# Kernel tuning notes

Measured on AMD Instinct MI355X. Metric: run time of the kernel, lower is better.

Reference implementation:

```python
import jax, jax.numpy as jnp
import numpy as np

OUT_F, IN_F = 4096, 4096
BITS = 4
B, S = 4, 2048


def setup_inputs() -> dict:
    key = jax.random.key(0)
    k_x, k_cb, k_rot, k_b, k_idx = jax.random.split(key, 5)
    x = jax.random.normal(k_x, (B, S, IN_F), dtype=jnp.float32)
    # per-coordinate codebook indices for each weight row (int, constant)
    indices = jax.random.randint(k_idx, (OUT_F, IN_F), 0, 2 ** BITS, dtype=jnp.int32)
    # scalar codebook with 2^bits levels
    codebook = jax.random.normal(k_cb, (2 ** BITS,), dtype=jnp.float32)
    # random rotation Pi (d x d); faithful math only needs it orthogonal-ish
    rotation_matrix = jax.random.normal(k_rot, (IN_F, IN_F), dtype=jnp.float32) / np.sqrt(IN_F)
    bias = jax.random.normal(k_b, (OUT_F,), dtype=jnp.float32)
    return {"x": x, "indices": indices, "codebook": codebook,
            "rotation_matrix": rotation_matrix, "bias": bias}


def reference(x, indices, codebook, rotation_matrix, bias):
    # Dequantize: look up codewords per coordinate in rotated space, then
    # undo the rotation: W = C[idx] @ Pi^T  -> [out_features, in_features]
    rotated = codebook[indices]                      # [O, D] gather
    weight = jnp.einsum('od,kd->ok', rotated, rotation_matrix)  # rotated @ Pi^T
    # F.linear(x, W, bias) = x @ W^T + bias
    out = jnp.einsum('bsd,od->bso', x, weight) + bias
    return out
```

## Files before the change

### kernel.cpp

```cpp
#include <hip/hip_runtime.h>
#include <hip/hip_bf16.h>


typedef __attribute__((ext_vector_type(8))) __bf16 bf16x8;
typedef __attribute__((ext_vector_type(4))) float f32x4;

#define GLOAD_LDS16(g, l)                                                        \
  __builtin_amdgcn_global_load_lds((__attribute__((address_space(1))) void*)(g), \
                                   (__attribute__((address_space(3))) void*)(l), \
                                   16, 0, 0)


__global__ __launch_bounds__(256) void cvt_f32_bf16(const float* __restrict__ in,
                                                    __hip_bfloat16* __restrict__ out, int n4) {
  int i = blockIdx.x * 256 + threadIdx.x;
  if (i >= n4) return;
  float4 v = *(const float4*)(in + (size_t)i * 4);
  union { __hip_bfloat16 h[4]; ushort4 u; } o;
  o.h[0] = __float2bfloat16(v.x);
  o.h[1] = __float2bfloat16(v.y);
  o.h[2] = __float2bfloat16(v.z);
  o.h[3] = __float2bfloat16(v.w);
  *(ushort4*)((unsigned short*)out + (size_t)i * 4) = o.u;
}

__global__ __launch_bounds__(256) void dequant_bf16(const int* __restrict__ idx,
                                                    const float* __restrict__ cb,
                                                    __hip_bfloat16* __restrict__ out, int n4) {
  __shared__ __hip_bfloat16 scb[16];
  if (threadIdx.x < 16) scb[threadIdx.x] = __float2bfloat16(cb[threadIdx.x]);
  __syncthreads();
  int i = blockIdx.x * 256 + threadIdx.x;
  if (i >= n4) return;
  int4 v = *(const int4*)(idx + (size_t)i * 4);
  union { __hip_bfloat16 h[4]; ushort4 u; } o;
  o.h[0] = scb[v.x & 15];
  o.h[1] = scb[v.y & 15];
  o.h[2] = scb[v.z & 15];
  o.h[3] = scb[v.w & 15];
  *(ushort4*)((unsigned short*)out + (size_t)i * 4) = o.u;
}


template <bool OUT_BF16>
__global__ __launch_bounds__(512, 2) void gemm256(const __hip_bfloat16* __restrict__ A,
                                                  const __hip_bfloat16* __restrict__ B,
                                                  void* __restrict__ Cv,
                                                  const float* __restrict__ bias,
                                                  int M, int N, int K) {
  __shared__ __align__(16) char smem[131072];

  const int nbn = N >> 8;
  const int nwg = (M >> 8) * nbn;
  const int bid0 = blockIdx.x;
  const int cpx = nwg >> 3;
  const int bid = (bid0 & 7) * cpx + (bid0 >> 3);
  const int m0 = (bid / nbn) << 8;
  const int n0 = (bid % nbn) << 8;

  const int tid = (int)threadIdx.x;
  const int lane = tid & 63;
  const int w = tid >> 6;
  const int wr = w >> 2;
  const int wc = w & 3;
  const int fr = lane & 15;
  const int fq = lane >> 4;

  const int srow = lane >> 3;
  const int scol = ((lane & 7) ^ srow) << 3;

  const __hip_bfloat16* Ab = A + (size_t)m0 * K;
  const __hip_bfloat16* Bb = B + (size_t)n0 * K;

  const int NT = K >> 6;

  f32x4 acc[8][4];
#pragma unroll
  for (int i = 0; i < 8; ++i)
#pragma unroll
    for (int j = 0; j < 4; ++j) acc[i][j] = (f32x4){0.f, 0.f, 0.f, 0.f};

  auto stage = [&](int s) {
    const int t = s >> 2, kind = s & 3;
    const __hip_bfloat16* g = (kind < 2) ? Ab : Bb;
    char* region = smem + ((kind < 2) ? 0 : 65536) + (t & 1) * 32768 + (kind & 1) * 16384;
    const int grow = (kind & 1) * 128 + w * 16 + srow;
    const int k0 = t << 6;
#pragma unroll
    for (int j = 0; j < 2; ++j)
      GLOAD_LDS16(g + (size_t)(grow + j * 8) * K + (k0 + scol), region + w * 2048 + j * 1024);
  };

  const int sw = (fr & 7) << 4;

  auto ldA = [&](int b, int mh, int mf, int kk) -> bf16x8 {
    const int row = wr * 128 + mh * 64 + mf * 16 + fr;
    const int byte = b * 32768 + row * 128 + ((kk * 64 + fq * 16) ^ sw);
    return *(const bf16x8*)(smem + byte);
  };
  auto ldB = [&](int b, int nf, int kk) -> bf16x8 {
    const int row = wc * 64 + nf * 16 + fr;
    const int byte = 65536 + b * 32768 + row * 128 + ((kk * 64 + fq * 16) ^ sw);
    return *(const bf16x8*)(smem + byte);
  };

  stage(0); stage(1); stage(2); stage(3);
  stage(6); stage(7);
  asm volatile("s_waitcnt vmcnt(4)" ::: "memory");
  __builtin_amdgcn_s_barrier();

  bf16x8 afA[4], afB[4], bk0[4], bk1[4];

  for (int T = 0; T < NT; ++T) {
    const int b = T & 1;
    const bool pf1 = (T + 1 < NT);
    const bool pf2 = (T + 2 < NT);

    if (pf1) stage(4 * (T + 1) + 0);
#pragma unroll
    for (int mf = 0; mf < 4; ++mf) afA[mf] = ldA(b, 0, mf, 0);
#pragma unroll
    for (int nf = 0; nf < 4; ++nf) bk0[nf] = ldB(b, nf, 0);
    __builtin_amdgcn_s_barrier();
    asm volatile("s_waitcnt lgkmcnt(0)");
    __builtin_amdgcn_sched_barrier(0);
#pragma unroll
    for (int mf = 0; mf < 4; ++mf) afB[mf] = ldA(b, 0, mf, 1);
#pragma unroll
    for (int nf = 0; nf < 4; ++nf) bk1[nf] = ldB(b, nf, 1);
    __builtin_amdgcn_s_setprio(1);
#pragma unroll
    for (int nf = 0; nf < 4; ++nf)
#pragma unroll
      for (int mf = 0; mf < 4; ++mf)
        acc[mf][nf] = __builtin_amdgcn_mfma_f32_16x16x32_bf16(afA[mf], bk0[nf], acc[mf][nf], 0, 0, 0);
    __builtin_amdgcn_s_setprio(0);
    __builtin_amdgcn_s_barrier();

    if (pf1) stage(4 * (T + 1) + 1);
    __builtin_amdgcn_s_barrier();
    asm volatile("s_waitcnt lgkmcnt(0)");
    __builtin_amdgcn_sched_barrier(0);
#pragma unroll
    for (int mf = 0; mf < 4; ++mf) afA[mf] = ldA(b, 1, mf, 0);
    __builtin_amdgcn_s_setprio(1);
#pragma unroll
    for (int nf = 0; nf < 4; ++nf)
#pragma unroll
      for (int mf = 0; mf < 4; ++mf)
        acc[mf][nf] = __builtin_amdgcn_mfma_f32_16x16x32_bf16(afB[mf], bk1[nf], acc[mf][nf], 0, 0, 0);
    __builtin_amdgcn_s_setprio(0);
    __builtin_amdgcn_s_barrier();

    if (pf2) stage(4 * (T + 2) + 2);
    __builtin_amdgcn_s_barrier();
    asm volatile("s_waitcnt lgkmcnt(0)");
    __builtin_amdgcn_sched_barrier(0);
#pragma unroll
    for (int mf = 0; mf < 4; ++mf) afB[mf] = ldA(b, 1, mf, 1);
    __builtin_amdgcn_s_setprio(1);
#pragma unroll
    for (int nf = 0; nf < 4; ++nf)
#pragma unroll
      for (int mf = 0; mf < 4; ++mf)
        acc[4 + mf][nf] = __builtin_amdgcn_mfma_f32_16x16x32_bf16(afA[mf], bk0[nf], acc[4 + mf][nf], 0, 0, 0);
    __builtin_amdgcn_s_setprio(0);
    __builtin_amdgcn_s_barrier();

    if (pf2) stage(4 * (T + 2) + 3);
    __builtin_amdgcn_s_barrier();
    asm volatile("s_waitcnt lgkmcnt(0)");
    __builtin_amdgcn_sched_barrier(0);
    __builtin_amdgcn_s_setprio(1);
#pragma unroll
    for (int nf = 0; nf < 4; ++nf)
#pragma unroll
      for (int mf = 0; mf < 4; ++mf)
        acc[4 + mf][nf] = __builtin_amdgcn_mfma_f32_16x16x32_bf16(afB[mf], bk1[nf], acc[4 + mf][nf], 0, 0, 0);
    __builtin_amdgcn_s_setprio(0);
    if (pf2) {
      asm volatile("s_waitcnt vmcnt(4)" ::: "memory");
    } else if (T + 2 == NT) {
      asm volatile("s_waitcnt vmcnt(0)" ::: "memory");
    }
    __builtin_amdgcn_s_barrier();
  }

  if constexpr (OUT_BF16) {
    __hip_bfloat16* C = (__hip_bfloat16*)Cv;
#pragma unroll
    for (int mi = 0; mi < 8; ++mi)
#pragma unroll
      for (int ni = 0; ni < 4; ++ni) {
        const size_t row = (size_t)(m0 + wr * 128 + (mi >> 2) * 64 + (mi & 3) * 16 + fq * 4);
        const int col = n0 + wc * 64 + ni * 16 + fr;
#pragma unroll
        for (int v = 0; v < 4; ++v) C[(row + v) * N + col] = __float2bfloat16(acc[mi][ni][v]);
      }
  } else {
    float* C = (float*)Cv;
    float bv[4];
#pragma unroll
    for (int ni = 0; ni < 4; ++ni) bv[ni] = bias[n0 + wc * 64 + ni * 16 + fr];
#pragma unroll
    for (int mi = 0; mi < 8; ++mi)
#pragma unroll
      for (int ni = 0; ni < 4; ++ni) {
        const size_t row = (size_t)(m0 + wr * 128 + (mi >> 2) * 64 + (mi & 3) * 16 + fq * 4);
        const int col = n0 + wc * 64 + ni * 16 + fr;
#pragma unroll
        for (int v = 0; v < 4; ++v) C[(row + v) * N + col] = acc[mi][ni][v] + bv[ni];
      }
  }
}


extern "C" void kernel_launch(void* const* d_in, const int* in_sizes, int n_in,
                              void* d_out, int out_size, void* d_ws, size_t ws_size,
                              hipStream_t stream) {
  const float* x = (const float*)d_in[0];
  const int* indices = (const int*)d_in[1];
  const float* codebook = (const float*)d_in[2];
  const float* rot = (const float*)d_in[3];
  const float* bias = (const float*)d_in[4];
  float* out = (float*)d_out;

  const int D = 4096, O = 4096;
  const int M = in_sizes[0] / D;

  char* ws = (char*)d_ws;
  __hip_bfloat16* Xb = (__hip_bfloat16*)ws;
  __hip_bfloat16* Rb = (__hip_bfloat16*)(ws + ((size_t)64 << 20));
  __hip_bfloat16* Wr = (__hip_bfloat16*)(ws + ((size_t)96 << 20));
  __hip_bfloat16* Wb = (__hip_bfloat16*)(ws + ((size_t)128 << 20));

  cvt_f32_bf16<<<(M * D / 4 + 255) / 256, 256, 0, stream>>>(x, Xb, M * D / 4);
  cvt_f32_bf16<<<(4096 * 4096 / 4 + 255) / 256, 256, 0, stream>>>(rot, Rb, 4096 * 4096 / 4);
  dequant_bf16<<<(4096 * 4096 / 4 + 255) / 256, 256, 0, stream>>>(indices, codebook, Wr,
                                                                  4096 * 4096 / 4);

  gemm256<true><<<dim3((O / 256) * (4096 / 256)), 512, 0, stream>>>(Wr, Rb, Wb, nullptr, O, 4096,
                                                                    D);
  gemm256<false><<<dim3((M / 256) * (O / 256)), 512, 0, stream>>>(Xb, Wb, out, bias, M, O, 4096);
}
```

Before: 446.2 us.

## Switch GEMM inner loop to 32x32x16 MFMA with restructured phase schedule

Replaces the 16x16x32 bf16 MFMA tiles with 32x32x16 MFMA instructions. Each wave's 128x64 sub-tile now uses 4x2 accumulators of 16 floats. The main loop is unrolled by two K-tiles into eight uniform phases that interleave LDS fragment loads, async global-to-LDS staging and MFMA blocks, and the epilogue is rewritten for the 32x32 output layout. Larger MFMAs need fewer LDS fragment reads per FLOP and fewer instructions. The risk is that the new schedule and prefetch wait counts could stall, and the unrolling assumes NT is even.

```diff
diff --git a/kernel.cpp b/kernel.cpp
--- a/kernel.cpp
+++ b/kernel.cpp
@@ -3,7 +3,7 @@
 
 
 typedef __attribute__((ext_vector_type(8))) __bf16 bf16x8;
-typedef __attribute__((ext_vector_type(4))) float f32x4;
+typedef __attribute__((ext_vector_type(16))) float f32x16;
 
 #define GLOAD_LDS16(g, l)                                                        \
   __builtin_amdgcn_global_load_lds((__attribute__((address_space(1))) void*)(g), \
@@ -63,8 +63,8 @@
   const int w = tid >> 6;
   const int wr = w >> 2;
   const int wc = w & 3;
-  const int fr = lane & 15;
-  const int fq = lane >> 4;
+  const int ln31 = lane & 31;
+  const int hi = lane >> 5;
 
   const int srow = lane >> 3;
   const int scol = ((lane & 7) ^ srow) << 3;
@@ -74,11 +74,11 @@
 
   const int NT = K >> 6;
 
-  f32x4 acc[8][4];
-#pragma unroll
-  for (int i = 0; i < 8; ++i)
-#pragma unroll
-    for (int j = 0; j < 4; ++j) acc[i][j] = (f32x4){0.f, 0.f, 0.f, 0.f};
+  f32x16 acc[4][2];
+#pragma unroll
+  for (int i = 0; i < 4; ++i)
+#pragma unroll
+    for (int j = 0; j < 2; ++j) acc[i][j] = (f32x16){};
 
   auto stage = [&](int s) {
     const int t = s >> 2, kind = s & 3;
@@ -91,17 +91,53 @@
       GLOAD_LDS16(g + (size_t)(grow + j * 8) * K + (k0 + scol), region + w * 2048 + j * 1024);
   };
 
-  const int sw = (fr & 7) << 4;
-
-  auto ldA = [&](int b, int mh, int mf, int kk) -> bf16x8 {
-    const int row = wr * 128 + mh * 64 + mf * 16 + fr;
-    const int byte = b * 32768 + row * 128 + ((kk * 64 + fq * 16) ^ sw);
+  const int sw = (lane & 7) << 4;
+
+  auto ldA32 = [&](int b, int mi, int ks) -> bf16x8 {
+    const int row = wr * 128 + mi * 32 + ln31;
+    const int byte = b * 32768 + row * 128 + ((ks * 32 + hi * 16) ^ sw);
     return *(const bf16x8*)(smem + byte);
   };
-  auto ldB = [&](int b, int nf, int kk) -> bf16x8 {
-    const int row = wc * 64 + nf * 16 + fr;
-    const int byte = 65536 + b * 32768 + row * 128 + ((kk * 64 + fq * 16) ^ sw);
+  auto ldB32 = [&](int b, int ni, int ks) -> bf16x8 {
+    const int row = wc * 64 + ni * 32 + ln31;
+    const int byte = 65536 + b * 32768 + row * 128 + ((ks * 32 + hi * 16) ^ sw);
     return *(const bf16x8*)(smem + byte);
+  };
+
+  bf16x8 af[2][2];
+  bf16x8 bk[2][2][2];
+
+  auto phase = [&](int BUF, int MH, int KH, int stage_s, int wait) {
+#pragma unroll
+    for (int mi2 = 0; mi2 < 2; ++mi2)
+#pragma unroll
+      for (int ks2 = 0; ks2 < 2; ++ks2) af[mi2][ks2] = ldA32(BUF, MH * 2 + mi2, KH * 2 + ks2);
+    if (MH == 0) {
+#pragma unroll
+      for (int ni = 0; ni < 2; ++ni)
+#pragma unroll
+        for (int ks2 = 0; ks2 < 2; ++ks2) bk[KH][ni][ks2] = ldB32(BUF, ni, KH * 2 + ks2);
+    }
+    if (stage_s >= 0) stage(stage_s);
+    __builtin_amdgcn_s_barrier();
+    asm volatile("s_waitcnt lgkmcnt(0)");
+    __builtin_amdgcn_sched_barrier(0);
+    __builtin_amdgcn_s_setprio(1);
+#pragma unroll
+    for (int ks2 = 0; ks2 < 2; ++ks2)
+#pragma unroll
+      for (int mi2 = 0; mi2 < 2; ++mi2)
+#pragma unroll
+        for (int ni = 0; ni < 2; ++ni)
+          acc[MH * 2 + mi2][ni] = __builtin_amdgcn_mfma_f32_32x32x16_bf16(
+              af[mi2][ks2], bk[KH][ni][ks2], acc[MH * 2 + mi2][ni], 0, 0, 0);
+    __builtin_amdgcn_s_setprio(0);
+    if (wait == 1) {
+      asm volatile("s_waitcnt vmcnt(4)" ::: "memory");
+    } else if (wait == 2) {
+      asm volatile("s_waitcnt vmcnt(0)" ::: "memory");
+    }
+    __builtin_amdgcn_s_barrier();
   };
 
   stage(0); stage(1); stage(2); stage(3);
@@ -109,107 +145,46 @@
   asm volatile("s_waitcnt vmcnt(4)" ::: "memory");
   __builtin_amdgcn_s_barrier();
 
-  bf16x8 afA[4], afB[4], bk0[4], bk1[4];
-
-  for (int T = 0; T < NT; ++T) {
-    const int b = T & 1;
-    const bool pf1 = (T + 1 < NT);
-    const bool pf2 = (T + 2 < NT);
-
-    if (pf1) stage(4 * (T + 1) + 0);
-#pragma unroll
-    for (int mf = 0; mf < 4; ++mf) afA[mf] = ldA(b, 0, mf, 0);
-#pragma unroll
-    for (int nf = 0; nf < 4; ++nf) bk0[nf] = ldB(b, nf, 0);
-    __builtin_amdgcn_s_barrier();
-    asm volatile("s_waitcnt lgkmcnt(0)");
-    __builtin_amdgcn_sched_barrier(0);
-#pragma unroll
-    for (int mf = 0; mf < 4; ++mf) afB[mf] = ldA(b, 0, mf, 1);
-#pragma unroll
-    for (int nf = 0; nf < 4; ++nf) bk1[nf] = ldB(b, nf, 1);
-    __builtin_amdgcn_s_setprio(1);
-#pragma unroll
-    for (int nf = 0; nf < 4; ++nf)
-#pragma unroll
-      for (int mf = 0; mf < 4; ++mf)
-        acc[mf][nf] = __builtin_amdgcn_mfma_f32_16x16x32_bf16(afA[mf], bk0[nf], acc[mf][nf], 0, 0, 0);
-    __builtin_amdgcn_s_setprio(0);
-    __builtin_amdgcn_s_barrier();
-
-    if (pf1) stage(4 * (T + 1) + 1);
-    __builtin_amdgcn_s_barrier();
-    asm volatile("s_waitcnt lgkmcnt(0)");
-    __builtin_amdgcn_sched_barrier(0);
-#pragma unroll
-    for (int mf = 0; mf < 4; ++mf) afA[mf] = ldA(b, 1, mf, 0);
-    __builtin_amdgcn_s_setprio(1);
-#pragma unroll
-    for (int nf = 0; nf < 4; ++nf)
-#pragma unroll
-      for (int mf = 0; mf < 4; ++mf)
-        acc[mf][nf] = __builtin_amdgcn_mfma_f32_16x16x32_bf16(afB[mf], bk1[nf], acc[mf][nf], 0, 0, 0);
-    __builtin_amdgcn_s_setprio(0);
-    __builtin_amdgcn_s_barrier();
-
-    if (pf2) stage(4 * (T + 2) + 2);
-    __builtin_amdgcn_s_barrier();
-    asm volatile("s_waitcnt lgkmcnt(0)");
-    __builtin_amdgcn_sched_barrier(0);
-#pragma unroll
-    for (int mf = 0; mf < 4; ++mf) afB[mf] = ldA(b, 1, mf, 1);
-    __builtin_amdgcn_s_setprio(1);
-#pragma unroll
-    for (int nf = 0; nf < 4; ++nf)
-#pragma unroll
-      for (int mf = 0; mf < 4; ++mf)
-        acc[4 + mf][nf] = __builtin_amdgcn_mfma_f32_16x16x32_bf16(afA[mf], bk0[nf], acc[4 + mf][nf], 0, 0, 0);
-    __builtin_amdgcn_s_setprio(0);
-    __builtin_amdgcn_s_barrier();
-
-    if (pf2) stage(4 * (T + 2) + 3);
-    __builtin_amdgcn_s_barrier();
-    asm volatile("s_waitcnt lgkmcnt(0)");
-    __builtin_amdgcn_sched_barrier(0);
-    __builtin_amdgcn_s_setprio(1);
-#pragma unroll
-    for (int nf = 0; nf < 4; ++nf)
-#pragma unroll
-      for (int mf = 0; mf < 4; ++mf)
-        acc[4 + mf][nf] = __builtin_amdgcn_mfma_f32_16x16x32_bf16(afB[mf], bk1[nf], acc[4 + mf][nf], 0, 0, 0);
-    __builtin_amdgcn_s_setprio(0);
-    if (pf2) {
-      asm volatile("s_waitcnt vmcnt(4)" ::: "memory");
-    } else if (T + 2 == NT) {
-      asm volatile("s_waitcnt vmcnt(0)" ::: "memory");
-    }
-    __builtin_amdgcn_s_barrier();
+  for (int E = 0; E < NT; E += 2) {
+    const bool pf2 = (E + 2 < NT);
+    phase(0, 0, 0, 4 * (E + 1) + 0, 0);
+    phase(0, 0, 1, 4 * (E + 1) + 1, 0);
+    phase(0, 1, 0, pf2 ? 4 * (E + 2) + 2 : -1, 0);
+    phase(0, 1, 1, pf2 ? 4 * (E + 2) + 3 : -1, pf2 ? 1 : 2);
+    phase(1, 0, 0, pf2 ? 4 * (E + 2) + 0 : -1, 0);
+    phase(1, 0, 1, pf2 ? 4 * (E + 2) + 1 : -1, 0);
+    phase(1, 1, 0, pf2 ? 4 * (E + 3) + 2 : -1, 0);
+    phase(1, 1, 1, pf2 ? 4 * (E + 3) + 3 : -1, pf2 ? 1 : 0);
   }
 
   if constexpr (OUT_BF16) {
     __hip_bfloat16* C = (__hip_bfloat16*)Cv;
 #pragma unroll
-    for (int mi = 0; mi < 8; ++mi)
-#pragma unroll
-      for (int ni = 0; ni < 4; ++ni) {
-        const size_t row = (size_t)(m0 + wr * 128 + (mi >> 2) * 64 + (mi & 3) * 16 + fq * 4);
-        const int col = n0 + wc * 64 + ni * 16 + fr;
-#pragma unroll
-        for (int v = 0; v < 4; ++v) C[(row + v) * N + col] = __float2bfloat16(acc[mi][ni][v]);
+    for (int mi = 0; mi < 4; ++mi)
+#pragma unroll
+      for (int ni = 0; ni < 2; ++ni) {
+        const int colg = n0 + wc * 64 + ni * 32 + ln31;
+#pragma unroll
+        for (int r = 0; r < 16; ++r) {
+          const int rowg = m0 + wr * 128 + mi * 32 + (r & 3) + 8 * (r >> 2) + 4 * hi;
+          C[(size_t)rowg * N + colg] = __float2bfloat16(acc[mi][ni][r]);
+        }
       }
   } else {
     float* C = (float*)Cv;
-    float bv[4];
-#pragma unroll
-    for (int ni = 0; ni < 4; ++ni) bv[ni] = bias[n0 + wc * 64 + ni * 16 + fr];
-#pragma unroll
-    for (int mi = 0; mi < 8; ++mi)
-#pragma unroll
-      for (int ni = 0; ni < 4; ++ni) {
-        const size_t row = (size_t)(m0 + wr * 128 + (mi >> 2) * 64 + (mi & 3) * 16 + fq * 4);
-        const int col = n0 + wc * 64 + ni * 16 + fr;
-#pragma unroll
-        for (int v = 0; v < 4; ++v) C[(row + v) * N + col] = acc[mi][ni][v] + bv[ni];
+    float bv[2];
+#pragma unroll
+    for (int ni = 0; ni < 2; ++ni) bv[ni] = bias[n0 + wc * 64 + ni * 32 + ln31];
+#pragma unroll
+    for (int mi = 0; mi < 4; ++mi)
+#pragma unroll
+      for (int ni = 0; ni < 2; ++ni) {
+        const int colg = n0 + wc * 64 + ni * 32 + ln31;
+#pragma unroll
+        for (int r = 0; r < 16; ++r) {
+          const int rowg = m0 + wr * 128 + mi * 32 + (r & 3) + 8 * (r >> 2) + 4 * hi;
+          C[(size_t)rowg * N + colg] = acc[mi][ni][r] + bv[ni];
+        }
       }
   }
 }
```

Measured after the change: 678.3 us. +52.0%, slower.
